# Kernel tuning notes

Measured on AMD Instinct MI355X. Metric: run time of the kernel, lower is better.

The kernel has to match this reference:

```python
import jax, jax.numpy as jnp
import numpy as np
from jax import lax

N_MAX = 350  # fixed adjacency size from the original module

def _conv(x, w, b):
    y = lax.conv_general_dilated(x, w, (1, 1), 'SAME',
                                 dimension_numbers=('NCHW', 'OIHW', 'NCHW'))
    return y + b[None, :, None, None]

def _maxpool2(x):
    return lax.reduce_window(x, -jnp.inf, lax.max, (1, 1, 2, 2), (1, 1, 2, 2), 'VALID')

def _lin(x, w, b):  # torch Linear: w [out,in]
    return x @ w.T + b

def setup_inputs() -> dict:
    key = jax.random.key(0)
    ks = jax.random.split(key, 24)
    B = 16
    images = jax.random.normal(ks[0], (B, 1, 256, 256), dtype=jnp.float32)
    # prefix masks: first n_b nodes valid, n_b in [2, 350]
    counts = jax.random.randint(ks[1], (B,), 2, N_MAX + 1)
    node_masks = jnp.arange(N_MAX)[None, :] < counts[:, None]
    def p(k, shape, s=0.02):
        return jax.random.normal(k, shape, dtype=jnp.float32) * s
    inp = {
        'images': images, 'node_masks': node_masks,
        # baseline CNN: 1->32->64->128->256, 3x3 convs
        'c1w': p(ks[2], (32, 1, 3, 3)),   'c1b': p(ks[3], (32,)),
        'c2w': p(ks[4], (64, 32, 3, 3)),  'c2b': p(ks[5], (64,)),
        'c3w': p(ks[6], (128, 64, 3, 3)), 'c3b': p(ks[7], (128,)),
        'c4w': p(ks[8], (256, 128, 3, 3)),'c4b': p(ks[9], (256,)),
        # node_detector: 256->512->700
        'nd1w': p(ks[10], (512, 256)), 'nd1b': p(ks[11], (512,)),
        'nd2w': p(ks[12], (N_MAX * 2, 512)), 'nd2b': p(ks[13], (N_MAX * 2,)),
        # count_predictor: 256->256->1
        'cp1w': p(ks[14], (256, 256)), 'cp1b': p(ks[15], (256,)),
        'cp2w': p(ks[16], (1, 256)),   'cp2b': p(ks[17], (1,)),
        # mlp_correction: 1->32->16->1
        'mc1w': p(ks[18], (32, 1)),  'mc1b': p(ks[19], (32,)),
        'mc2w': p(ks[20], (16, 32)), 'mc2b': p(ks[21], (16,)),
        'mc3w': p(ks[22], (1, 16)),  'mc3b': p(ks[23], (1,)),
    }
    return inp

def reference(images, node_masks,
              c1w, c1b, c2w, c2b, c3w, c3b, c4w, c4b,
              nd1w, nd1b, nd2w, nd2b,
              cp1w, cp1b, cp2w, cp2b,
              mc1w, mc1b, mc2w, mc2b, mc3w, mc3b):
    B = images.shape[0]
    relu = jax.nn.relu
    # CNN encoder (baseline)
    x = _maxpool2(relu(_conv(images, c1w, c1b)))
    x = _maxpool2(relu(_conv(x, c2w, c2b)))
    x = _maxpool2(relu(_conv(x, c3w, c3b)))
    x = relu(_conv(x, c4w, c4b))
    feat = jnp.mean(x, axis=(2, 3))  # AdaptiveAvgPool2d((1,1)) -> [B,256]
    # node detector (dropout is identity in eval)
    coords = _lin(relu(_lin(feat, nd1w, nd1b)), nd2w, nd2b).reshape(B, N_MAX, 2)
    # count predictor
    count = _lin(relu(_lin(feat, cp1w, cp1b)), cp2w, cp2b)[:, 0]
    # cosine similarity over all 350 slots (row-wise normalize is mask-independent)
    cn = coords / jnp.maximum(jnp.linalg.norm(coords, axis=-1, keepdims=True), 1e-12)
    sim = jnp.einsum('bnd,bmd->bnm', cn, cn)  # [B,350,350]
    # pointwise 1->32->16->1 MLP correction + sigmoid
    h1 = relu(sim[..., None] * mc1w[:, 0] + mc1b)          # [B,N,N,32]
    h2 = relu(jnp.einsum('bnmk,jk->bnmj', h1, mc2w) + mc2b)  # [B,N,N,16]
    corr = jax.nn.sigmoid(jnp.einsum('bnmj,oj->bnmo', h2, mc3w)[..., 0] + mc3b[0])
    # scatter-pad into fixed 350x350: with prefix masks this is elementwise pair masking
    m = node_masks.astype(corr.dtype)
    pair = m[:, :, None] * m[:, None, :]
    valid = (node_masks.sum(-1) > 1).astype(corr.dtype)  # n_nodes<=1 -> zero adj
    adjacency = corr * pair * valid[:, None, None]
    return (coords, adjacency, count)
```

## Files before the change

kernel.cpp:

```cpp
#include <hip/hip_runtime.h>
#include <hip/hip_bf16.h>
#include <math.h>

typedef __hip_bfloat16 bf16;
typedef __attribute__((ext_vector_type(8))) short short8;
typedef __attribute__((ext_vector_type(4))) float f32x4;

__device__ __forceinline__ bf16 f2b(float v){ return __float2bfloat16(v); }
__device__ __forceinline__ float ldf(float v){ return v; }
__device__ __forceinline__ float ldf(bf16 v){ return __bfloat162float(v); }
__device__ __forceinline__ unsigned short fbits(float v){
  __hip_bfloat16 h = __float2bfloat16(v);
  return *reinterpret_cast<unsigned short*>(&h);
}
__device__ __forceinline__ float dot4(float4 a, float4 b){
  return fmaf(a.x,b.x, fmaf(a.y,b.y, fmaf(a.z,b.z, a.w*b.w)));
}

__global__ void k_prep(const float* __restrict__ c2w, const float* __restrict__ c3w,
                       const float* __restrict__ c4w, bf16* __restrict__ wt2,
                       bf16* __restrict__ wt3, bf16* __restrict__ wt4,
                       const float* __restrict__ w1, const float* __restrict__ b1,
                       const float* __restrict__ w2, const float* __restrict__ b2,
                       const float* __restrict__ w3, const float* __restrict__ b3,
                       float* __restrict__ lut){
  int bid = blockIdx.x;
  if(bid < 1512){
    int e = bid*256 + threadIdx.x;
    const float* w; bf16* wt; int OC, IC;
    if(e < 18432){ w = c2w; wt = wt2; OC = 64;  IC = 32; }
    else if(e < 92160){ e -= 18432; w = c3w; wt = wt3; OC = 128; IC = 64; }
    else { e -= 92160; w = c4w; wt = wt4; OC = 256; IC = 128; }
    int ic = e % IC; int t2 = e / IC; int oc = t2 % OC; int tap = t2 / OC;
    wt[e] = f2b(w[(oc*IC + ic)*9 + tap]);
  } else {
    int e = (bid-1512)*256 + threadIdx.x;
    float s = -1.f + (2.f/4095.f)*e;
    float h1[32];
    #pragma unroll
    for(int k=0;k<32;k++) h1[k] = fmaxf(fmaf(s, w1[k], b1[k]), 0.f);
    float a3 = b3[0];
    #pragma unroll
    for(int j=0;j<16;j++){
      float t = b2[j];
      #pragma unroll
      for(int k=0;k<32;k++) t = fmaf(h1[k], w2[j*32+k], t);
      a3 = fmaf(fmaxf(t,0.f), w3[j], a3);
    }
    lut[e] = 1.f/(1.f + expf(-a3));
  }
}

__global__ __launch_bounds__(256) void k_conv1(const float* __restrict__ img,
                        const float* __restrict__ w, const float* __restrict__ bias,
                        bf16* __restrict__ out){
  __shared__ float Wl[288], Bl[32];
  int tid = threadIdx.x;
  for(int t=tid; t<288; t+=256) Wl[t] = w[t];
  if(tid<32) Bl[tid] = bias[tid];
  __syncthreads();
  int idx = blockIdx.x*256 + tid;
  int ox = idx & 127, oy = (idx>>7)&127, b = idx>>14;
  const float* ip = img + (size_t)b*65536;
  int y0 = oy*2-1, x0 = ox*2-1;
  float patch[4][4];
  #pragma unroll
  for(int py=0;py<4;py++){
    int y=y0+py; bool yok = (unsigned)y<256u;
    #pragma unroll
    for(int px=0;px<4;px++){
      int x=x0+px;
      patch[py][px] = (yok && (unsigned)x<256u) ? ip[y*256+x] : 0.f;
    }
  }
  unsigned u[16];
  #pragma unroll
  for(int og=0; og<16; og++){
    unsigned short hb[2];
    #pragma unroll
    for(int h=0; h<2; h++){
      int oc = og*2 + h;
      const float* wj = &Wl[oc*9];
      float best = 0.f;
      #pragma unroll
      for(int py=0;py<2;py++)
      #pragma unroll
      for(int px=0;px<2;px++){
        float a = Bl[oc];
        #pragma unroll
        for(int ky=0;ky<3;ky++)
        #pragma unroll
        for(int kx=0;kx<3;kx++)
          a = fmaf(wj[ky*3+kx], patch[py+ky][px+kx], a);
        best = fmaxf(best, a);
      }
      hb[h] = fbits(best);
    }
    u[og] = (unsigned)hb[0] | ((unsigned)hb[1] << 16);
  }
  uint4* dst = (uint4*)(out + (size_t)idx*32);
  dst[0] = make_uint4(u[0],u[1],u[2],u[3]);
  dst[1] = make_uint4(u[4],u[5],u[6],u[7]);
  dst[2] = make_uint4(u[8],u[9],u[10],u[11]);
  dst[3] = make_uint4(u[12],u[13],u[14],u[15]);
}

template<int L>
__global__ __launch_bounds__(256) void k_convmfma(const bf16* __restrict__ in,
                      const bf16* __restrict__ wt, const float* __restrict__ bias,
                      bf16* __restrict__ out, float* __restrict__ partial2){
  constexpr int IC   = L==2?32:(L==3?64:128);
  constexpr int OC   = L==2?64:(L==3?128:256);
  constexpr int HW   = L==2?128:(L==3?64:32);
  constexpr int POOL = L==4?0:1;
  constexpr int WNF  = L==4?2:4;
  constexpr int IC8  = IC/8;
  constexpr int SM   = (IC8-1)&7;
  constexpr int KC   = IC/32;
  constexpr int XT   = HW;
  constexpr int ROWC = (XT+2)*IC8;
  __shared__ short8 T[4*ROWC];

  int bid = blockIdx.x;
  int b, py, bt = 0;
  if(L==4){ b = bid>>5; py = (bid>>1)&15; bt = bid&1; }
  else if(L==3){ b = bid>>5; py = bid&31; }
  else { b = bid>>6; py = bid&63; }

  int tid = threadIdx.x;
  int w = tid>>6, l15 = tid&15, lhi = (tid>>4)&3;

  int mbase, nbase;
  if(L==2){ mbase = w*32; nbase = 0; }
  else if(L==3){ mbase = (w&1)*32; nbase = (w>>1)*64; }
  else { mbase = 0; nbase = bt*128 + w*32; }

  for(int c=tid; c<4*2*IC8; c+=256){
    int r = c/(2*IC8), rem = c%(2*IC8);
    int X = (rem>=IC8)?(XT+1):0;
    int k = rem%IC8;
    short8 z = {0,0,0,0,0,0,0,0};
    T[(r*(XT+2)+X)*IC8 + k] = z;
  }
  for(int c=tid; c<4*XT*IC8; c+=256){
    int r = c/(XT*IC8), rem = c%(XT*IC8);
    int x = rem/IC8, k = rem%IC8;
    int gy = 2*py - 1 + r;
    short8 v = {0,0,0,0,0,0,0,0};
    if((unsigned)gy < (unsigned)HW)
      v = *(const short8*)(in + (((size_t)b*HW + gy)*XT + x)*IC + k*8);
    int X = x+1;
    T[(r*(XT+2)+X)*IC8 + (k ^ (X&SM))] = v;
  }
  __syncthreads();

  float bv[WNF];
  #pragma unroll
  for(int n=0;n<WNF;n++) bv[n] = bias[nbase + n*16 + l15];
  f32x4 acc[2][2][WNF];
  #pragma unroll
  for(int r=0;r<2;r++)
  #pragma unroll
  for(int m=0;m<2;m++)
  #pragma unroll
  for(int n=0;n<WNF;n++){
    acc[r][m][n][0]=bv[n]; acc[r][m][n][1]=bv[n];
    acc[r][m][n][2]=bv[n]; acc[r][m][n][3]=bv[n];
  }

  const short8* wt8 = (const short8*)wt;
  #pragma unroll
  for(int tap=0; tap<9; tap++){
    const int dy = tap/3 - 1, dx = tap%3 - 1;
    #pragma unroll
    for(int kc=0; kc<KC; kc++){
      short8 Bf[WNF];
      #pragma unroll
      for(int n=0;n<WNF;n++){
        int oc = nbase + n*16 + l15;
        Bf[n] = wt8[(size_t)(tap*OC + oc)*IC8 + kc*4 + lhi];
      }
      short8 Af[2][2];
      #pragma unroll
      for(int r=0;r<2;r++)
      #pragma unroll
      for(int m=0;m<2;m++){
        int X = mbase + m*16 + l15 + dx + 1;
        int rs = r + dy + 1;
        Af[r][m] = T[(rs*(XT+2)+X)*IC8 + ((kc*4+lhi) ^ (X&SM))];
      }
      #pragma unroll
      for(int r=0;r<2;r++)
      #pragma unroll
      for(int m=0;m<2;m++)
      #pragma unroll
      for(int n=0;n<WNF;n++)
        acc[r][m][n] = __builtin_amdgcn_mfma_f32_16x16x32_bf16(Af[r][m], Bf[n], acc[r][m][n], 0,0,0);
    }
  }

  if(POOL){
    constexpr int HP = HW/2;
    #pragma unroll
    for(int m=0;m<2;m++)
    #pragma unroll
    for(int n=0;n<WNF;n++){
      int oc = nbase + n*16 + l15;
      #pragma unroll
      for(int t=0;t<2;t++){
        float v = fmaxf(fmaxf(acc[0][m][n][2*t], acc[0][m][n][2*t+1]),
                        fmaxf(acc[1][m][n][2*t], acc[1][m][n][2*t+1]));
        v = fmaxf(v, 0.f);
        int xp = (mbase + m*16)/2 + lhi*2 + t;
        out[(((size_t)b*HP + py)*HP + xp)*OC + oc] = f2b(v);
      }
    }
  } else {
    #pragma unroll
    for(int n=0;n<WNF;n++){
      float p = 0.f;
      #pragma unroll
      for(int r=0;r<2;r++)
      #pragma unroll
      for(int m=0;m<2;m++)
      #pragma unroll
      for(int j=0;j<4;j++)
        p += fmaxf(acc[r][m][n][j], 0.f);
      p += __shfl_xor(p, 16);
      p += __shfl_xor(p, 32);
      if(lhi == 0)
        partial2[((size_t)(b*16+py))*256 + nbase + n*16 + l15] = p;
    }
  }
}

__global__ __launch_bounds__(256) void k_headA(const float* __restrict__ partial2,
                      const float* __restrict__ nd1w, const float* __restrict__ nd1b,
                      const float* __restrict__ cp1w, const float* __restrict__ cp1b,
                      float* __restrict__ h512, float* __restrict__ h256){
  __shared__ float F[256];
  int b = blockIdx.x / 192, blk = blockIdx.x % 192;
  int tid = threadIdx.x;
  float s = 0.f;
  #pragma unroll
  for(int q=0;q<16;q++) s += partial2[((size_t)(b*16+q))*256 + tid];
  F[tid] = s * (1.f/1024.f);
  __syncthreads();
  int w = tid>>6, lane = tid&63;
  int o = blk*4 + w;
  float4 xv = ((const float4*)F)[lane];
  const float* wrow; float bb; float* dst; int oo;
  if(o < 512){ wrow = nd1w + (size_t)o*256; bb = nd1b[o]; dst = h512 + b*512 + o; }
  else { oo = o - 512; wrow = cp1w + (size_t)oo*256; bb = cp1b[oo]; dst = h256 + b*256 + oo; }
  float a = dot4(((const float4*)wrow)[lane], xv);
  #pragma unroll
  for(int off=32; off>0; off>>=1) a += __shfl_xor(a, off);
  if(lane==0) *dst = fmaxf(a + bb, 0.f);
}

__global__ __launch_bounds__(256) void k_headB(const float* __restrict__ h512,
                      const float* __restrict__ h256,
                      const float* __restrict__ nd2w, const float* __restrict__ nd2b,
                      const float* __restrict__ cp2w, const float* __restrict__ cp2b,
                      float* __restrict__ coordsOut, float* __restrict__ countOut){
  int b = blockIdx.x / 176, blk = blockIdx.x % 176;
  int tid = threadIdx.x;
  int w = tid>>6, lane = tid&63;
  int o = blk*4 + w;
  if(o > 700) return;
  float a;
  if(o < 700){
    const float4* xp = (const float4*)(h512 + b*512);
    const float4* wp = (const float4*)(nd2w + (size_t)o*512);
    a = dot4(wp[lane], xp[lane]) + dot4(wp[lane+64], xp[lane+64]);
  } else {
    const float4* xp = (const float4*)(h256 + b*256);
    const float4* wp = (const float4*)cp2w;
    a = dot4(wp[lane], xp[lane]);
  }
  #pragma unroll
  for(int off=32; off>0; off>>=1) a += __shfl_xor(a, off);
  if(lane==0){
    if(o < 700) coordsOut[b*700 + o] = a + nd2b[o];
    else        countOut[b] = a + cp2b[0];
  }
}

__device__ __forceinline__ int mask_mode(const void* p){
  unsigned w0 = ((const unsigned*)p)[0];
  unsigned w1 = ((const unsigned*)p)[1];
  if(w0 == 1u) return (w1 == 0u) ? 4 : 0;
  if(w0 == 0x3F800000u) return 3;
  unsigned short h0 = (unsigned short)(w0 & 0xFFFFu);
  if(h0 == 0x3F80u || h0 == 0x3C00u) return 2;
  return 1;
}
__device__ __forceinline__ int mask_get(const void* p, int i, int mode){
  switch(mode){
    case 0: return ((const int*)p)[i] != 0;
    case 1: return ((const unsigned char*)p)[i] != 0;
    case 2: return ((const unsigned short*)p)[i] != 0;
    case 3: return ((const float*)p)[i] != 0.f;
    default: return ((const long long*)p)[i] != 0ll;
  }
}

__global__ __launch_bounds__(256) void k_adj(const float* __restrict__ coords,
                      const void* __restrict__ masks, const float* __restrict__ lut,
                      float* __restrict__ out){
  int idx = blockIdx.x*256 + threadIdx.x;
  if(idx >= 16*350*350) return;
  int m  = idx % 350;
  int t2 = idx / 350;
  int n  = t2 % 350;
  int b  = t2 / 350;
  int mode = mask_mode(masks);
  float o = 0.f;
  if(mask_get(masks, b*350+1, mode) &&
     mask_get(masks, b*350+n, mode) && mask_get(masks, b*350+m, mode)){
    float2 a = ((const float2*)coords)[b*350+n];
    float2 c = ((const float2*)coords)[b*350+m];
    float dn = fmaxf(sqrtf(fmaf(a.x,a.x, a.y*a.y)), 1e-12f);
    float dm = fmaxf(sqrtf(fmaf(c.x,c.x, c.y*c.y)), 1e-12f);
    float s = fmaf(a.x, c.x, a.y*c.y) / (dn*dm);
    float u = (s + 1.f) * 2047.5f;
    u = fminf(fmaxf(u, 0.f), 4095.f);
    int i = min((int)u, 4094);
    float fr = u - (float)i;
    float l0 = lut[i], l1 = lut[i+1];
    o = fmaf(l1 - l0, fr, l0);
  }
  out[idx] = o;
}

extern "C" void kernel_launch(void* const* d_in, const int* in_sizes, int n_in,
                              void* d_out, int out_size, void* d_ws, size_t ws_size,
                              hipStream_t stream){
  const float* images = (const float*)d_in[0];
  const void*  masks  = d_in[1];
  const float *c1w=(const float*)d_in[2],  *c1b=(const float*)d_in[3];
  const float *c2w=(const float*)d_in[4],  *c2b=(const float*)d_in[5];
  const float *c3w=(const float*)d_in[6],  *c3b=(const float*)d_in[7];
  const float *c4w=(const float*)d_in[8],  *c4b=(const float*)d_in[9];
  const float *nd1w=(const float*)d_in[10],*nd1b=(const float*)d_in[11];
  const float *nd2w=(const float*)d_in[12],*nd2b=(const float*)d_in[13];
  const float *cp1w=(const float*)d_in[14],*cp1b=(const float*)d_in[15];
  const float *cp2w=(const float*)d_in[16],*cp2b=(const float*)d_in[17];
  const float *mc1w=(const float*)d_in[18],*mc1b=(const float*)d_in[19];
  const float *mc2w=(const float*)d_in[20],*mc2b=(const float*)d_in[21];
  const float *mc3w=(const float*)d_in[22],*mc3b=(const float*)d_in[23];
  float* out = (float*)d_out;

  char* W = (char*)d_ws;
  float* partial2 = (float*)W;
  float* h512     = (float*)(W + 262144);
  float* h256     = (float*)(W + 294912);
  float* lut      = (float*)(W + 311296);
  bf16*  wt2 = (bf16*)(W + 524288);
  bf16*  wt3 = (bf16*)(W + 561152);
  bf16*  wt4 = (bf16*)(W + 708608);
  bf16*  x1 = (bf16*)(W + 2097152);
  bf16*  x2 = (bf16*)(W + 2097152 + 16777216);
  bf16*  x3 = (bf16*)(W + 2097152);

  float* coordsOut = out;
  float* adjOut    = out + 11200;
  float* countOut  = out + 11200 + 1960000;

  k_prep<<<1528, 256, 0, stream>>>(c2w, c3w, c4w, wt2, wt3, wt4,
                                   mc1w, mc1b, mc2w, mc2b, mc3w, mc3b, lut);
  k_conv1<<<1024, 256, 0, stream>>>(images, c1w, c1b, x1);
  k_convmfma<2><<<1024, 256, 0, stream>>>(x1, wt2, c2b, x2, nullptr);
  k_convmfma<3><<<512, 256, 0, stream>>>(x2, wt3, c3b, x3, nullptr);
  k_convmfma<4><<<512, 256, 0, stream>>>(x3, wt4, c4b, nullptr, partial2);
  k_headA<<<3072, 256, 0, stream>>>(partial2, nd1w, nd1b, cp1w, cp1b, h512, h256);
  k_headB<<<2816, 256, 0, stream>>>(h512, h256, nd2w, nd2b, cp2w, cp2b,
                                    coordsOut, countOut);
  k_adj<<<7657, 256, 0, stream>>>(coordsOut, masks, lut, adjOut);
}
```

Before: 109.0 us.

## Fuse conv1 with prep, split conv3/conv4 along x, vectorize adjacency stores

Merges the weight-transpose/LUT prep kernel and conv1 into one launch to remove a kernel boundary. Splits conv3 and conv4 blocks along the x dimension (doubling the grid to 1024 blocks) with a smaller per-warp M tile and a new LDS swizzle, so more blocks can be resident. The pooled partial-sum buffer and the workspace offsets are resized to match. The adjacency kernel now computes four outputs per thread and writes them with one float4 store, which adds per-element div/mod work.

```diff
diff --git a/kernel.cpp b/kernel.cpp
--- a/kernel.cpp
+++ b/kernel.cpp
@@ -17,49 +17,51 @@
   return fmaf(a.x,b.x, fmaf(a.y,b.y, fmaf(a.z,b.z, a.w*b.w)));
 }
 
-__global__ void k_prep(const float* __restrict__ c2w, const float* __restrict__ c3w,
-                       const float* __restrict__ c4w, bf16* __restrict__ wt2,
-                       bf16* __restrict__ wt3, bf16* __restrict__ wt4,
-                       const float* __restrict__ w1, const float* __restrict__ b1,
-                       const float* __restrict__ w2, const float* __restrict__ b2,
-                       const float* __restrict__ w3, const float* __restrict__ b3,
-                       float* __restrict__ lut){
+__global__ __launch_bounds__(256) void k_c1prep(const float* __restrict__ img,
+                        const float* __restrict__ c1w, const float* __restrict__ c1b,
+                        bf16* __restrict__ x1,
+                        const float* __restrict__ c2w, const float* __restrict__ c3w,
+                        const float* __restrict__ c4w, bf16* __restrict__ wt2,
+                        bf16* __restrict__ wt3, bf16* __restrict__ wt4,
+                        const float* __restrict__ w1, const float* __restrict__ b1,
+                        const float* __restrict__ w2, const float* __restrict__ b2,
+                        const float* __restrict__ w3, const float* __restrict__ b3,
+                        float* __restrict__ lut){
   int bid = blockIdx.x;
-  if(bid < 1512){
-    int e = bid*256 + threadIdx.x;
-    const float* w; bf16* wt; int OC, IC;
-    if(e < 18432){ w = c2w; wt = wt2; OC = 64;  IC = 32; }
-    else if(e < 92160){ e -= 18432; w = c3w; wt = wt3; OC = 128; IC = 64; }
-    else { e -= 92160; w = c4w; wt = wt4; OC = 256; IC = 128; }
-    int ic = e % IC; int t2 = e / IC; int oc = t2 % OC; int tap = t2 / OC;
-    wt[e] = f2b(w[(oc*IC + ic)*9 + tap]);
-  } else {
-    int e = (bid-1512)*256 + threadIdx.x;
-    float s = -1.f + (2.f/4095.f)*e;
-    float h1[32];
-    #pragma unroll
-    for(int k=0;k<32;k++) h1[k] = fmaxf(fmaf(s, w1[k], b1[k]), 0.f);
-    float a3 = b3[0];
-    #pragma unroll
-    for(int j=0;j<16;j++){
-      float t = b2[j];
-      #pragma unroll
-      for(int k=0;k<32;k++) t = fmaf(h1[k], w2[j*32+k], t);
-      a3 = fmaf(fmaxf(t,0.f), w3[j], a3);
-    }
-    lut[e] = 1.f/(1.f + expf(-a3));
-  }
-}
-
-__global__ __launch_bounds__(256) void k_conv1(const float* __restrict__ img,
-                        const float* __restrict__ w, const float* __restrict__ bias,
-                        bf16* __restrict__ out){
+  int tid = threadIdx.x;
+  if(bid >= 1024){
+    int pb = bid - 1024;
+    if(pb < 1512){
+      int e = pb*256 + tid;
+      const float* w; bf16* wt; int OC, IC;
+      if(e < 18432){ w = c2w; wt = wt2; OC = 64;  IC = 32; }
+      else if(e < 92160){ e -= 18432; w = c3w; wt = wt3; OC = 128; IC = 64; }
+      else { e -= 92160; w = c4w; wt = wt4; OC = 256; IC = 128; }
+      int ic = e % IC; int t2 = e / IC; int oc = t2 % OC; int tap = t2 / OC;
+      wt[e] = f2b(w[(oc*IC + ic)*9 + tap]);
+    } else {
+      int e = (pb-1512)*256 + tid;
+      float s = -1.f + (2.f/4095.f)*e;
+      float h1[32];
+      #pragma unroll
+      for(int k=0;k<32;k++) h1[k] = fmaxf(fmaf(s, w1[k], b1[k]), 0.f);
+      float a3 = b3[0];
+      #pragma unroll
+      for(int j=0;j<16;j++){
+        float t = b2[j];
+        #pragma unroll
+        for(int k=0;k<32;k++) t = fmaf(h1[k], w2[j*32+k], t);
+        a3 = fmaf(fmaxf(t,0.f), w3[j], a3);
+      }
+      lut[e] = 1.f/(1.f + expf(-a3));
+    }
+    return;
+  }
   __shared__ float Wl[288], Bl[32];
-  int tid = threadIdx.x;
-  for(int t=tid; t<288; t+=256) Wl[t] = w[t];
-  if(tid<32) Bl[tid] = bias[tid];
+  for(int t=tid; t<288; t+=256) Wl[t] = c1w[t];
+  if(tid<32) Bl[tid] = c1b[tid];
   __syncthreads();
-  int idx = blockIdx.x*256 + tid;
+  int idx = bid*256 + tid;
   int ox = idx & 127, oy = (idx>>7)&127, b = idx>>14;
   const float* ip = img + (size_t)b*65536;
   int y0 = oy*2-1, x0 = ox*2-1;
@@ -98,7 +100,7 @@
     }
     u[og] = (unsigned)hb[0] | ((unsigned)hb[1] << 16);
   }
-  uint4* dst = (uint4*)(out + (size_t)idx*32);
+  uint4* dst = (uint4*)(x1 + (size_t)idx*32);
   dst[0] = make_uint4(u[0],u[1],u[2],u[3]);
   dst[1] = make_uint4(u[4],u[5],u[6],u[7]);
   dst[2] = make_uint4(u[8],u[9],u[10],u[11]);
@@ -113,55 +115,47 @@
   constexpr int OC   = L==2?64:(L==3?128:256);
   constexpr int HW   = L==2?128:(L==3?64:32);
   constexpr int POOL = L==4?0:1;
-  constexpr int WNF  = L==4?2:4;
+  constexpr int WNF  = L==2?4:2;
+  constexpr int MF   = L==4?1:2;
+  constexpr int XB   = L==2?128:(L==3?32:16);
   constexpr int IC8  = IC/8;
   constexpr int SM   = (IC8-1)&7;
   constexpr int KC   = IC/32;
-  constexpr int XT   = HW;
-  constexpr int ROWC = (XT+2)*IC8;
-  __shared__ short8 T[4*ROWC];
+  constexpr int XS   = XB+2;
+  __shared__ short8 T[4*XS*IC8];
 
   int bid = blockIdx.x;
-  int b, py, bt = 0;
-  if(L==4){ b = bid>>5; py = (bid>>1)&15; bt = bid&1; }
-  else if(L==3){ b = bid>>5; py = bid&31; }
-  else { b = bid>>6; py = bid&63; }
+  int b, py, xh = 0, nq = 0;
+  if(L==2){ b = bid>>6; py = bid&63; }
+  else if(L==3){ b = bid>>6; py = (bid>>1)&31; xh = bid&1; }
+  else { b = bid>>6; py = (bid>>2)&15; xh = (bid>>1)&1; nq = bid&1; }
 
   int tid = threadIdx.x;
   int w = tid>>6, l15 = tid&15, lhi = (tid>>4)&3;
-
-  int mbase, nbase;
-  if(L==2){ mbase = w*32; nbase = 0; }
-  else if(L==3){ mbase = (w&1)*32; nbase = (w>>1)*64; }
-  else { mbase = 0; nbase = bt*128 + w*32; }
-
-  for(int c=tid; c<4*2*IC8; c+=256){
-    int r = c/(2*IC8), rem = c%(2*IC8);
-    int X = (rem>=IC8)?(XT+1):0;
-    int k = rem%IC8;
-    short8 z = {0,0,0,0,0,0,0,0};
-    T[(r*(XT+2)+X)*IC8 + k] = z;
-  }
-  for(int c=tid; c<4*XT*IC8; c+=256){
-    int r = c/(XT*IC8), rem = c%(XT*IC8);
-    int x = rem/IC8, k = rem%IC8;
+  int mbase = (L==2)? w*32 : 0;
+  int nbase = (L==2)? 0 : nq*128 + w*32;
+
+  const int gx0 = xh*XB - 1;
+  for(int t=tid; t<4*XS*IC8; t+=256){
+    int r = t/(XS*IC8), rem = t%(XS*IC8);
+    int X = rem/IC8, k = rem%IC8;
     int gy = 2*py - 1 + r;
+    int gx = gx0 + X;
     short8 v = {0,0,0,0,0,0,0,0};
-    if((unsigned)gy < (unsigned)HW)
-      v = *(const short8*)(in + (((size_t)b*HW + gy)*XT + x)*IC + k*8);
-    int X = x+1;
-    T[(r*(XT+2)+X)*IC8 + (k ^ (X&SM))] = v;
+    if((unsigned)gy < (unsigned)HW && (unsigned)gx < (unsigned)HW)
+      v = *(const short8*)(in + (((size_t)b*HW + gy)*HW + gx)*IC + k*8);
+    T[(r*XS+X)*IC8 + (k ^ ((X ^ (X>>2)) & SM))] = v;
   }
   __syncthreads();
 
   float bv[WNF];
   #pragma unroll
   for(int n=0;n<WNF;n++) bv[n] = bias[nbase + n*16 + l15];
-  f32x4 acc[2][2][WNF];
+  f32x4 acc[2][MF][WNF];
   #pragma unroll
   for(int r=0;r<2;r++)
   #pragma unroll
-  for(int m=0;m<2;m++)
+  for(int m=0;m<MF;m++)
   #pragma unroll
   for(int n=0;n<WNF;n++){
     acc[r][m][n][0]=bv[n]; acc[r][m][n][1]=bv[n];
@@ -180,19 +174,19 @@
         int oc = nbase + n*16 + l15;
         Bf[n] = wt8[(size_t)(tap*OC + oc)*IC8 + kc*4 + lhi];
       }
-      short8 Af[2][2];
+      short8 Af[2][MF];
       #pragma unroll
       for(int r=0;r<2;r++)
       #pragma unroll
-      for(int m=0;m<2;m++){
+      for(int m=0;m<MF;m++){
         int X = mbase + m*16 + l15 + dx + 1;
         int rs = r + dy + 1;
-        Af[r][m] = T[(rs*(XT+2)+X)*IC8 + ((kc*4+lhi) ^ (X&SM))];
+        Af[r][m] = T[(rs*XS+X)*IC8 + ((kc*4+lhi) ^ ((X ^ (X>>2)) & SM))];
       }
       #pragma unroll
       for(int r=0;r<2;r++)
       #pragma unroll
-      for(int m=0;m<2;m++)
+      for(int m=0;m<MF;m++)
       #pragma unroll
       for(int n=0;n<WNF;n++)
         acc[r][m][n] = __builtin_amdgcn_mfma_f32_16x16x32_bf16(Af[r][m], Bf[n], acc[r][m][n], 0,0,0);
@@ -202,7 +196,7 @@
   if(POOL){
     constexpr int HP = HW/2;
     #pragma unroll
-    for(int m=0;m<2;m++)
+    for(int m=0;m<MF;m++)
     #pragma unroll
     for(int n=0;n<WNF;n++){
       int oc = nbase + n*16 + l15;
@@ -211,7 +205,7 @@
         float v = fmaxf(fmaxf(acc[0][m][n][2*t], acc[0][m][n][2*t+1]),
                         fmaxf(acc[1][m][n][2*t], acc[1][m][n][2*t+1]));
         v = fmaxf(v, 0.f);
-        int xp = (mbase + m*16)/2 + lhi*2 + t;
+        int xp = (xh*XB + mbase + m*16)/2 + lhi*2 + t;
         out[(((size_t)b*HP + py)*HP + xp)*OC + oc] = f2b(v);
       }
     }
@@ -222,14 +216,12 @@
       #pragma unroll
       for(int r=0;r<2;r++)
       #pragma unroll
-      for(int m=0;m<2;m++)
-      #pragma unroll
       for(int j=0;j<4;j++)
-        p += fmaxf(acc[r][m][n][j], 0.f);
+        p += fmaxf(acc[r][0][n][j], 0.f);
       p += __shfl_xor(p, 16);
       p += __shfl_xor(p, 32);
       if(lhi == 0)
-        partial2[((size_t)(b*16+py))*256 + nbase + n*16 + l15] = p;
+        partial2[((size_t)((b*16+py)*2+xh))*256 + nbase + n*16 + l15] = p;
     }
   }
 }
@@ -243,7 +235,7 @@
   int tid = threadIdx.x;
   float s = 0.f;
   #pragma unroll
-  for(int q=0;q<16;q++) s += partial2[((size_t)(b*16+q))*256 + tid];
+  for(int q=0;q<32;q++) s += partial2[((size_t)(b*32+q))*256 + tid];
   F[tid] = s * (1.f/1024.f);
   __syncthreads();
   int w = tid>>6, lane = tid&63;
@@ -308,29 +300,34 @@
 __global__ __launch_bounds__(256) void k_adj(const float* __restrict__ coords,
                       const void* __restrict__ masks, const float* __restrict__ lut,
                       float* __restrict__ out){
-  int idx = blockIdx.x*256 + threadIdx.x;
-  if(idx >= 16*350*350) return;
-  int m  = idx % 350;
-  int t2 = idx / 350;
-  int n  = t2 % 350;
-  int b  = t2 / 350;
+  int t4 = blockIdx.x*256 + threadIdx.x;
+  if(t4 >= 490000) return;
+  int base = t4*4;
+  int b = base / 122500;
+  int rem = base % 122500;
   int mode = mask_mode(masks);
-  float o = 0.f;
-  if(mask_get(masks, b*350+1, mode) &&
-     mask_get(masks, b*350+n, mode) && mask_get(masks, b*350+m, mode)){
-    float2 a = ((const float2*)coords)[b*350+n];
-    float2 c = ((const float2*)coords)[b*350+m];
-    float dn = fmaxf(sqrtf(fmaf(a.x,a.x, a.y*a.y)), 1e-12f);
-    float dm = fmaxf(sqrtf(fmaf(c.x,c.x, c.y*c.y)), 1e-12f);
-    float s = fmaf(a.x, c.x, a.y*c.y) / (dn*dm);
-    float u = (s + 1.f) * 2047.5f;
-    u = fminf(fmaxf(u, 0.f), 4095.f);
-    int i = min((int)u, 4094);
-    float fr = u - (float)i;
-    float l0 = lut[i], l1 = lut[i+1];
-    o = fmaf(l1 - l0, fr, l0);
-  }
-  out[idx] = o;
+  int valid = mask_get(masks, b*350+1, mode);
+  float res[4];
+  #pragma unroll
+  for(int e=0;e<4;e++){
+    int n = (rem+e)/350, m = (rem+e)%350;
+    float o = 0.f;
+    if(valid && mask_get(masks, b*350+n, mode) && mask_get(masks, b*350+m, mode)){
+      float2 a = ((const float2*)coords)[b*350+n];
+      float2 c = ((const float2*)coords)[b*350+m];
+      float dn = fmaxf(sqrtf(fmaf(a.x,a.x, a.y*a.y)), 1e-12f);
+      float dm = fmaxf(sqrtf(fmaf(c.x,c.x, c.y*c.y)), 1e-12f);
+      float s = fmaf(a.x, c.x, a.y*c.y) / (dn*dm);
+      float u = (s + 1.f) * 2047.5f;
+      u = fminf(fmaxf(u, 0.f), 4095.f);
+      int i = min((int)u, 4094);
+      float fr = u - (float)i;
+      float l0 = lut[i], l1 = lut[i+1];
+      o = fmaf(l1 - l0, fr, l0);
+    }
+    res[e] = o;
+  }
+  *(float4*)(out + base) = make_float4(res[0], res[1], res[2], res[3]);
 }
 
 extern "C" void kernel_launch(void* const* d_in, const int* in_sizes, int n_in,
@@ -353,12 +350,12 @@
 
   char* W = (char*)d_ws;
   float* partial2 = (float*)W;
-  float* h512     = (float*)(W + 262144);
-  float* h256     = (float*)(W + 294912);
-  float* lut      = (float*)(W + 311296);
-  bf16*  wt2 = (bf16*)(W + 524288);
-  bf16*  wt3 = (bf16*)(W + 561152);
-  bf16*  wt4 = (bf16*)(W + 708608);
+  float* h512     = (float*)(W + 524288);
+  float* h256     = (float*)(W + 557056);
+  float* lut      = (float*)(W + 573440);
+  bf16*  wt2 = (bf16*)(W + 589824);
+  bf16*  wt3 = (bf16*)(W + 655360);
+  bf16*  wt4 = (bf16*)(W + 819200);
   bf16*  x1 = (bf16*)(W + 2097152);
   bf16*  x2 = (bf16*)(W + 2097152 + 16777216);
   bf16*  x3 = (bf16*)(W + 2097152);
@@ -367,14 +364,14 @@
   float* adjOut    = out + 11200;
   float* countOut  = out + 11200 + 1960000;
 
-  k_prep<<<1528, 256, 0, stream>>>(c2w, c3w, c4w, wt2, wt3, wt4,
-                                   mc1w, mc1b, mc2w, mc2b, mc3w, mc3b, lut);
-  k_conv1<<<1024, 256, 0, stream>>>(images, c1w, c1b, x1);
+  k_c1prep<<<2552, 256, 0, stream>>>(images, c1w, c1b, x1,
+                                     c2w, c3w, c4w, wt2, wt3, wt4,
+                                     mc1w, mc1b, mc2w, mc2b, mc3w, mc3b, lut);
   k_convmfma<2><<<1024, 256, 0, stream>>>(x1, wt2, c2b, x2, nullptr);
-  k_convmfma<3><<<512, 256, 0, stream>>>(x2, wt3, c3b, x3, nullptr);
-  k_convmfma<4><<<512, 256, 0, stream>>>(x3, wt4, c4b, nullptr, partial2);
+  k_convmfma<3><<<1024, 256, 0, stream>>>(x2, wt3, c3b, x3, nullptr);
+  k_convmfma<4><<<1024, 256, 0, stream>>>(x3, wt4, c4b, nullptr, partial2);
   k_headA<<<3072, 256, 0, stream>>>(partial2, nd1w, nd1b, cp1w, cp1b, h512, h256);
   k_headB<<<2816, 256, 0, stream>>>(h512, h256, nd2w, nd2b, cp2w, cp2b,
                                     coordsOut, countOut);
-  k_adj<<<7657, 256, 0, stream>>>(coordsOut, masks, lut, adjOut);
-}
+  k_adj<<<1915, 256, 0, stream>>>(coordsOut, masks, lut, adjOut);
+}
```

Result: slower. 120.4 us (+10.4%).
